# Kernel tuning notes

Measured on AMD Instinct MI355X. Metric: run time of the kernel, lower is better.

Reference implementation:

```python
import jax, jax.numpy as jnp
import numpy as np

B, N, D, H, TV, COND, BLK = 2, 1024, 1024, 16, 256, 1024, 16
HD = D // H  # 64
S = 2 * N    # total sequence [xt|x0]
EPS = 1e-5


def _ln(x, w):
    # bd3lm LayerNorm: no bias, weight multiply after normalization
    mu = jnp.mean(x, axis=-1, keepdims=True)
    var = jnp.mean(jnp.square(x - mu), axis=-1, keepdims=True)
    return (x - mu) * jax.lax.rsqrt(var + EPS) * w


def _rotate_half(u):
    u1, u2 = jnp.split(u, 2, axis=-1)
    return jnp.concatenate([-u2, u1], axis=-1)


def _apply_rotary(qkv, cos, sin):
    # qkv: (B, n, 3, H, HD); cos/sin: (1, n, 3, 1, HD) with identity on the v slot
    return qkv * cos + _rotate_half(qkv) * sin


def setup_inputs() -> dict:
    key = jax.random.key(0)
    ks = jax.random.split(key, 20)
    inp = {}
    inp['x'] = jax.random.normal(ks[0], (B, S, D), jnp.float32)
    inp['c'] = jax.random.normal(ks[1], (B, COND), jnp.float32)
    inp['encoder_out'] = jax.random.normal(ks[2], (B, TV, D), jnp.float32)
    # encoder padding mask: True = valid
    lengths = jax.random.randint(ks[3], (B,), TV // 2, TV + 1)
    inp['encoder_mask'] = jnp.arange(TV)[None, :] < lengths[:, None]
    # BD3LM block-causal mask over [xt|x0], shape (2N, 2N)
    bt = jnp.arange(N) // BLK
    M11 = bt[:, None] == bt[None, :]   # xt attends xt within same block
    M12 = bt[None, :] < bt[:, None]    # xt attends x0 of strictly earlier blocks
    M21 = jnp.zeros((N, N), bool)      # x0 does not attend xt
    M22 = bt[None, :] <= bt[:, None]   # x0 attends x0 block-causally
    inp['mask'] = jnp.concatenate([
        jnp.concatenate([M11, M12], axis=1),
        jnp.concatenate([M21, M22], axis=1)], axis=0)
    # rotary tables (SEDD-style), identity on v slot
    inv_freq = 1.0 / (10000.0 ** (jnp.arange(0, HD, 2, dtype=jnp.float32) / HD))
    freqs = jnp.outer(jnp.arange(N, dtype=jnp.float32), inv_freq)  # (N, HD/2)
    emb = jnp.concatenate([freqs, freqs], axis=-1)                 # (N, HD)
    cqk, sqk = jnp.cos(emb), jnp.sin(emb)
    inp['cos'] = jnp.stack([cqk, cqk, jnp.ones_like(cqk)], axis=1)[None, :, :, None, :]
    inp['sin'] = jnp.stack([sqk, sqk, jnp.zeros_like(sqk)], axis=1)[None, :, :, None, :]
    # parameters (torch Linear convention: W is (out, in), y = x @ W.T)
    sc = 0.02
    inp['ln1_w'] = jnp.ones((D,), jnp.float32)
    inp['W_qkv'] = jax.random.normal(ks[4], (3 * D, D), jnp.float32) * sc
    inp['W_attn_out'] = jax.random.normal(ks[5], (D, D), jnp.float32) * sc
    inp['ca_ln_w'] = jnp.ones((D,), jnp.float32)
    inp['ca_Wq'] = jax.random.normal(ks[6], (D, D), jnp.float32) * sc
    inp['ca_Wkv'] = jax.random.normal(ks[7], (2 * D, D), jnp.float32) * sc
    inp['ca_Wo'] = jax.random.normal(ks[8], (D, D), jnp.float32) * sc
    inp['ln2_w'] = jnp.ones((D,), jnp.float32)
    inp['W_mlp1'] = jax.random.normal(ks[9], (4 * D, D), jnp.float32) * sc
    inp['b_mlp1'] = jnp.zeros((4 * D,), jnp.float32)
    inp['W_mlp2'] = jax.random.normal(ks[10], (D, 4 * D), jnp.float32) * sc
    inp['b_mlp2'] = jnp.zeros((D,), jnp.float32)
    # adaLN (zero-init in the module; use small random weights for a non-trivial baseline)
    inp['W_ada'] = jax.random.normal(ks[11], (6 * D, COND), jnp.float32) * sc
    inp['b_ada'] = jax.random.normal(ks[12], (6 * D,), jnp.float32) * sc
    return inp


def _forward(x, c, encoder_out, encoder_mask, mask, cos, sin, ln1_w, W_qkv,
             W_attn_out, ca_ln_w, ca_Wq, ca_Wkv, ca_Wo, ln2_w, W_mlp1, b_mlp1,
             W_mlp2, b_mlp2, W_ada, b_ada):
    inv_sqrt_d = 1.0 / jnp.sqrt(jnp.float32(HD))
    ada = c @ W_ada.T + b_ada
    sh_msa, sc_msa, g_msa, sh_mlp, sc_mlp, g_mlp = [
        a[:, None, :] for a in jnp.split(ada, 6, axis=-1)]
    x_skip = x
    x_norm = _ln(x, ln1_w) * (1.0 + sc_msa) + sh_msa
    # qkv + rotary applied separately to xt and x0 halves (same positions 0..N-1)
    qkv = (x_norm @ W_qkv.T).reshape(B, S, 3, H, HD)
    qkv = jnp.concatenate([
        _apply_rotary(qkv[:, :N], cos, sin),
        _apply_rotary(qkv[:, N:], cos, sin)], axis=1)
    q, k, v = qkv[:, :, 0], qkv[:, :, 1], qkv[:, :, 2]  # (B, S, H, HD)
    # block-causal self-attention
    scores = jnp.einsum('bqhd,bkhd->bhqk', q, k) * inv_sqrt_d
    scores = jnp.where(mask[None, None, :, :], scores, jnp.finfo(scores.dtype).min)
    attn = jax.nn.softmax(scores, axis=-1)
    x_attn = jnp.einsum('bhqk,bkhd->bqhd', attn, v).reshape(B, S, D)
    # fused bias-dropout-add-scale (inference: scale * x + residual)
    x = g_msa * (x_attn @ W_attn_out.T) + x_skip
    # cross-attention to visual features
    res = x
    xn = _ln(x, ca_ln_w)
    qc = (xn @ ca_Wq.T).reshape(B, S, H, HD)
    kv = (encoder_out @ ca_Wkv.T).reshape(B, TV, 2, H, HD)
    kc, vc = kv[:, :, 0], kv[:, :, 1]
    cs = jnp.einsum('bqhd,bkhd->bhqk', qc, kc) * inv_sqrt_d
    cs = jnp.where(encoder_mask[:, None, None, :], cs, jnp.finfo(cs.dtype).min)
    ca = jax.nn.softmax(cs, axis=-1)
    co = jnp.einsum('bhqk,bkhd->bqhd', ca, vc).reshape(B, S, D)
    x = res + co @ ca_Wo.T
    # adaLN-modulated MLP (GELU tanh)
    h = _ln(x, ln2_w) * (1.0 + sc_mlp) + sh_mlp
    h = jax.nn.gelu(h @ W_mlp1.T + b_mlp1, approximate=True)
    return g_mlp * (h @ W_mlp2.T + b_mlp2) + x


def reference(x, c, encoder_out, encoder_mask, mask, cos, sin, ln1_w, W_qkv,
              W_attn_out, ca_ln_w, ca_Wq, ca_Wkv, ca_Wo, ln2_w, W_mlp1, b_mlp1,
              W_mlp2, b_mlp2, W_ada, b_ada):
    return _forward(x, c, encoder_out, encoder_mask, mask, cos, sin, ln1_w,
                    W_qkv, W_attn_out, ca_ln_w, ca_Wq, ca_Wkv, ca_Wo, ln2_w,
                    W_mlp1, b_mlp1, W_mlp2, b_mlp2, W_ada, b_ada)
```

## Files before the change

kernel.cpp:

```cpp
#include <hip/hip_runtime.h>
#include <hip/hip_bf16.h>

typedef __bf16 bf16x8 __attribute__((ext_vector_type(8)));
typedef __bf16 bf16x4 __attribute__((ext_vector_type(4)));
typedef float f32x4 __attribute__((ext_vector_type(4)));

typedef const __attribute__((address_space(1))) unsigned int* gas_t;
typedef __attribute__((address_space(3))) unsigned int* las_t;

__device__ __forceinline__ void gl_lds16(const void* g, void* l) {
    __builtin_amdgcn_global_load_lds((gas_t)g, (las_t)l, 16, 0, 0);
}

__device__ __forceinline__ float gelu_f(float u) {
    return u / (1.f + __expf(-1.5957691216057308f * (u + 0.044715f * u * u * u)));
}

struct CastArgs {
    const float4* src[8];
    __bf16* dst[8];
    int n4[8];
};
__global__ __launch_bounds__(256) void castmulti(CastArgs a) {
    int seg = blockIdx.y;
    const float4* src = a.src[seg];
    __bf16* dst = a.dst[seg];
    int n4 = a.n4[seg];
    for (int i = blockIdx.x * 256 + threadIdx.x; i < n4; i += 512 * 256) {
        float4 v = src[i];
        bf16x4 o;
        o[0] = (__bf16)v.x; o[1] = (__bf16)v.y; o[2] = (__bf16)v.z; o[3] = (__bf16)v.w;
        *(bf16x4*)(dst + (size_t)i * 4) = o;
    }
}

__global__ __launch_bounds__(256) void ada_kernel(const float* __restrict__ c, const float* __restrict__ W,
                                                  const float* __restrict__ bias, float* __restrict__ ada) {
    int o = blockIdx.x * 4 + (threadIdx.x >> 6);
    int lane = threadIdx.x & 63;
    int b = o / 6144, n = o % 6144;
    const float* cr = c + b * 1024;
    const float* wr = W + (size_t)n * 1024;
    float s = 0.f;
    #pragma unroll
    for (int i = 0; i < 16; ++i) s += cr[lane + i * 64] * wr[lane + i * 64];
    #pragma unroll
    for (int off = 1; off < 64; off <<= 1) s += __shfl_xor(s, off, 64);
    if (lane == 0) ada[o] = s + bias[n];
}

__global__ __launch_bounds__(256) void ln_kernel(const float* __restrict__ x, const float* __restrict__ w,
                                                 const float* __restrict__ ada, int sc_off, int sh_off,
                                                 int has_mod, __bf16* __restrict__ out) {
    int m = blockIdx.x;
    int b = m >> 11;
    int t = threadIdx.x;
    const float* xr = x + (size_t)m * 1024;
    float4 v = *(const float4*)(xr + t * 4);
    float s = v.x + v.y + v.z + v.w;
    float sq = v.x * v.x + v.y * v.y + v.z * v.z + v.w * v.w;
    #pragma unroll
    for (int off = 1; off < 64; off <<= 1) { s += __shfl_xor(s, off, 64); sq += __shfl_xor(sq, off, 64); }
    __shared__ float red[8];
    int wv = t >> 6, lane = t & 63;
    if (lane == 0) { red[wv] = s; red[4 + wv] = sq; }
    __syncthreads();
    s = red[0] + red[1] + red[2] + red[3];
    sq = red[4] + red[5] + red[6] + red[7];
    float mu = s * (1.f / 1024.f);
    float var = sq * (1.f / 1024.f) - mu * mu;
    float rs = rsqrtf(var + 1e-5f);
    const float* sc = ada + b * 6144 + sc_off;
    const float* sh = ada + b * 6144 + sh_off;
    float vv[4] = {v.x, v.y, v.z, v.w};
    #pragma unroll
    for (int i = 0; i < 4; ++i) {
        int d = t * 4 + i;
        float val = (vv[i] - mu) * rs * w[d];
        if (has_mod) val = val * (1.f + sc[d]) + sh[d];
        out[(size_t)m * 1024 + d] = (__bf16)val;
    }
}

__global__ __launch_bounds__(256) void rotary_kernel(const __bf16* __restrict__ qkv,
                                                     const float* __restrict__ cosp, const float* __restrict__ sinp,
                                                     __bf16* __restrict__ q, __bf16* __restrict__ k,
                                                     __bf16* __restrict__ v) {
    int m = blockIdx.y;
    int col = blockIdx.x * 256 + threadIdx.x;
    int tt = col >> 10;
    int hd = col & 1023;
    int h = hd >> 6, d = hd & 63;
    int b = m >> 11, s = m & 2047;
    int p = s & 1023;
    float u = (float)qkv[(size_t)m * 3072 + col];
    float res;
    if (tt < 2) {
        float cs = cosp[p * 192 + tt * 64 + d];
        float sn = sinp[p * 192 + tt * 64 + d];
        float prt = (float)qkv[(size_t)m * 3072 + (col ^ 32)];
        float rot = (d < 32) ? -prt : prt;
        res = u * cs + rot * sn;
        if (tt == 0) res *= 0.125f;
    } else {
        res = u;
    }
    size_t oi = ((size_t)(b * 16 + h) * 2048 + s) * 64 + d;
    __bf16* dst = (tt == 0) ? q : (tt == 1) ? k : v;
    dst[oi] = (__bf16)res;
}

__global__ __launch_bounds__(512) void gemm512(
    const __bf16* __restrict__ A, const __bf16* __restrict__ Bw,
    void* __restrict__ Cout, float* __restrict__ part,
    int M, int N, int K, int ksplit,
    const float* __restrict__ bias,
    const float* __restrict__ gate,
    const float* __restrict__ resid,
    int do_gelu, int out_bf16, float scale) {
    __shared__ __align__(16) __bf16 As[128 * 32];
    __shared__ __align__(16) __bf16 Bs[128 * 32];
    int t = threadIdx.x;
    int wv = t >> 6, lane = t & 63;
    int lrow = lane & 15, quad = lane >> 4;
    int m0 = blockIdx.y * 128, n0 = blockIdx.x * 128;
    int Ks = K / ksplit;
    int kbase = blockIdx.z * Ks;
    int wm = (wv >> 1) * 32, wn = (wv & 1) * 64;
    f32x4 acc[2][4] = {};
    const __bf16* Ag = A + (size_t)(m0 + wv * 16 + (lane >> 2)) * K + kbase + (lane & 3) * 8;
    const __bf16* Bg = Bw + (size_t)(n0 + wv * 16 + (lane >> 2)) * K + kbase + (lane & 3) * 8;
    __bf16* Asw = As + wv * 512;
    __bf16* Bsw = Bs + wv * 512;
    for (int k0 = 0; k0 < Ks; k0 += 32) {
        gl_lds16(Ag + k0, Asw);
        gl_lds16(Bg + k0, Bsw);
        __syncthreads();
        bf16x8 af[2], bfr[4];
        #pragma unroll
        for (int i = 0; i < 2; ++i) af[i] = *(const bf16x8*)(As + (wm + i * 16 + lrow) * 32 + quad * 8);
        #pragma unroll
        for (int j = 0; j < 4; ++j) bfr[j] = *(const bf16x8*)(Bs + (wn + j * 16 + lrow) * 32 + quad * 8);
        #pragma unroll
        for (int i = 0; i < 2; ++i)
            #pragma unroll
            for (int j = 0; j < 4; ++j)
                acc[i][j] = __builtin_amdgcn_mfma_f32_16x16x32_bf16(af[i], bfr[j], acc[i][j], 0, 0, 0);
        __syncthreads();
    }
    if (ksplit > 1) {
        float* pp = part + (size_t)blockIdx.z * M * N;
        #pragma unroll
        for (int i = 0; i < 2; ++i)
            #pragma unroll
            for (int j = 0; j < 4; ++j)
                #pragma unroll
                for (int r = 0; r < 4; ++r) {
                    int gm = m0 + wm + i * 16 + quad * 4 + r;
                    int gn = n0 + wn + j * 16 + lrow;
                    pp[(size_t)gm * N + gn] = acc[i][j][r] * scale;
                }
        return;
    }
    #pragma unroll
    for (int i = 0; i < 2; ++i) {
        #pragma unroll
        for (int j = 0; j < 4; ++j) {
            #pragma unroll
            for (int r = 0; r < 4; ++r) {
                int gm = m0 + wm + i * 16 + quad * 4 + r;
                int gn = n0 + wn + j * 16 + lrow;
                float val = acc[i][j][r] * scale;
                if (bias) val += bias[gn];
                if (do_gelu) val = gelu_f(val);
                if (gate) val *= gate[(gm >> 11) * 6144 + gn];
                if (resid) val += resid[(size_t)gm * N + gn];
                if (out_bf16) ((__bf16*)Cout)[(size_t)gm * N + gn] = (__bf16)val;
                else ((float*)Cout)[(size_t)gm * N + gn] = val;
            }
        }
    }
}

__global__ __launch_bounds__(256) void reduce2(
    const float4* __restrict__ p0, const float4* __restrict__ p1,
    const float* __restrict__ bias, const float* __restrict__ gate,
    const float* __restrict__ resid, float* __restrict__ out, int n4tot) {
    int i = blockIdx.x * 256 + threadIdx.x;
    if (i >= n4tot) return;
    float4 a = p0[i], b = p1[i];
    int idx = i * 4;
    int n = idx & 1023;
    int bb = idx >> 21;
    float4 bs = *(const float4*)(bias + n);
    float4 g = *(const float4*)(gate + bb * 6144 + n);
    float4 rr = ((const float4*)resid)[i];
    float4 o;
    o.x = g.x * (a.x + b.x + bs.x) + rr.x;
    o.y = g.y * (a.y + b.y + bs.y) + rr.y;
    o.z = g.z * (a.z + b.z + bs.z) + rr.z;
    o.w = g.w * (a.w + b.w + bs.w) + rr.w;
    ((float4*)out)[i] = o;
}

__global__ __launch_bounds__(256) void attn_kernel(
    const __bf16* __restrict__ qp, const __bf16* __restrict__ kp, const __bf16* __restrict__ vp,
    __bf16* __restrict__ op, const void* __restrict__ emask,
    int Sk, int mode,
    long qB, long qH, int qR,
    long kB, long kH, int kR,
    long vB, long vH, int vR,
    long oB, long oH, int oR) {
    __shared__ __bf16 Qs[64][72];
    __shared__ __bf16 Ks[64][72];
    __shared__ __bf16 Vt[64][72];
    __shared__ __bf16 Ps[4][16][72];
    int bh = blockIdx.y;
    int b = bh >> 4, h = bh & 15;
    int s0 = blockIdx.x * 64;
    int t = threadIdx.x;
    int wv = t >> 6, lane = t & 63;
    int lrow = lane & 15, quad = lane >> 4;
    const __bf16* qbase = qp + (size_t)b * qB + (size_t)h * qH;
    const __bf16* kbase = kp + (size_t)b * kB + (size_t)h * kH;
    const __bf16* vbase = vp + (size_t)b * vB + (size_t)h * vH;

    #pragma unroll
    for (int rep = 0; rep < 2; ++rep) {
        int g = t + rep * 256;
        int row = g >> 3, sg = g & 7;
        *(uint4*)(&Qs[row][sg * 8]) = *(const uint4*)(qbase + (size_t)(s0 + row) * qR + sg * 8);
    }
    bool m_is_i32 = false;
    if (mode == 1) m_is_i32 = (((const unsigned char*)emask)[1] == 0);

    float mrun[4], lrun[4];
    #pragma unroll
    for (int r = 0; r < 4; ++r) { mrun[r] = -1e30f; lrun[r] = 0.f; }
    f32x4 oacc[4] = {};

    int nt;
    if (mode == 1) nt = Sk >> 6;
    else nt = (s0 < 1024) ? (s0 / 64 + 2) : ((s0 - 1024) / 64 + 1);

    for (int ti = 0; ti < nt; ++ti) {
        int kb;
        if (mode == 1) kb = ti * 64;
        else if (s0 < 1024) kb = (ti == 0) ? s0 : 1024 + (ti - 1) * 64;
        else kb = 1024 + ti * 64;
        __syncthreads();
        #pragma unroll
        for (int rep = 0; rep < 2; ++rep) {
            int g = t + rep * 256;
            int row = g >> 3, sg = g & 7;
            *(uint4*)(&Ks[row][sg * 8]) = *(const uint4*)(kbase + (size_t)(kb + row) * kR + sg * 8);
        }
        {
            int j2 = (t & 31) * 2, dc = t >> 5;
            bf16x8 va = *(const bf16x8*)(vbase + (size_t)(kb + j2) * vR + dc * 8);
            bf16x8 vb2 = *(const bf16x8*)(vbase + (size_t)(kb + j2 + 1) * vR + dc * 8);
            #pragma unroll
            for (int i = 0; i < 8; ++i) {
                Vt[dc * 8 + i][j2] = va[i];
                Vt[dc * 8 + i][j2 + 1] = vb2[i];
            }
        }
        __syncthreads();
        f32x4 sacc[4] = {};
        #pragma unroll
        for (int ks = 0; ks < 64; ks += 32) {
            bf16x8 aq = *(const bf16x8*)(&Qs[wv * 16 + lrow][ks + quad * 8]);
            #pragma unroll
            for (int cc = 0; cc < 4; ++cc) {
                bf16x8 bk = *(const bf16x8*)(&Ks[cc * 16 + lrow][ks + quad * 8]);
                sacc[cc] = __builtin_amdgcn_mfma_f32_16x16x32_bf16(aq, bk, sacc[cc], 0, 0, 0);
            }
        }
        #pragma unroll
        for (int cc = 0; cc < 4; ++cc) {
            int kg = kb + cc * 16 + lrow;
            if (mode == 1) {
                bool visc = m_is_i32 ? (((const int*)emask)[b * Sk + kg] != 0)
                                     : (((const unsigned char*)emask)[b * Sk + kg] != 0);
                if (!visc) {
                    #pragma unroll
                    for (int r = 0; r < 4; ++r) sacc[cc][r] = -1e30f;
                }
            } else {
                #pragma unroll
                for (int r = 0; r < 4; ++r) {
                    int qg = s0 + wv * 16 + quad * 4 + r;
                    bool qh = qg < 1024, kh = kg < 1024;
                    bool vis;
                    if (qh && kh) vis = (qg >> 4) == (kg >> 4);
                    else if (qh) vis = ((kg - 1024) >> 4) < (qg >> 4);
                    else if (kh) vis = false;
                    else vis = ((kg - 1024) >> 4) <= ((qg - 1024) >> 4);
                    if (!vis) sacc[cc][r] = -1e30f;
                }
            }
        }
        #pragma unroll
        for (int r = 0; r < 4; ++r) {
            float mt = fmaxf(fmaxf(sacc[0][r], sacc[1][r]), fmaxf(sacc[2][r], sacc[3][r]));
            #pragma unroll
            for (int off = 1; off < 16; off <<= 1) mt = fmaxf(mt, __shfl_xor(mt, off, 64));
            float mnew = fmaxf(mrun[r], mt);
            float alpha = __expf(mrun[r] - mnew);
            float psum = 0.f;
            #pragma unroll
            for (int cc = 0; cc < 4; ++cc) {
                float pv = __expf(sacc[cc][r] - mnew);
                sacc[cc][r] = pv;
                psum += pv;
            }
            #pragma unroll
            for (int off = 1; off < 16; off <<= 1) psum += __shfl_xor(psum, off, 64);
            lrun[r] = lrun[r] * alpha + psum;
            mrun[r] = mnew;
            #pragma unroll
            for (int cc = 0; cc < 4; ++cc) oacc[cc][r] *= alpha;
            #pragma unroll
            for (int cc = 0; cc < 4; ++cc)
                Ps[wv][quad * 4 + r][cc * 16 + lrow] = (__bf16)sacc[cc][r];
        }
        __syncthreads();
        #pragma unroll
        for (int ks = 0; ks < 64; ks += 32) {
            bf16x8 ap = *(const bf16x8*)(&Ps[wv][lrow][ks + quad * 8]);
            #pragma unroll
            for (int cc = 0; cc < 4; ++cc) {
                bf16x8 bv = *(const bf16x8*)(&Vt[cc * 16 + lrow][ks + quad * 8]);
                oacc[cc] = __builtin_amdgcn_mfma_f32_16x16x32_bf16(ap, bv, oacc[cc], 0, 0, 0);
            }
        }
    }
    __bf16* obase = op + (size_t)b * oB + (size_t)h * oH;
    #pragma unroll
    for (int cc = 0; cc < 4; ++cc) {
        #pragma unroll
        for (int r = 0; r < 4; ++r) {
            int qg = s0 + wv * 16 + quad * 4 + r;
            obase[(size_t)qg * oR + cc * 16 + lrow] = (__bf16)(oacc[cc][r] / lrun[r]);
        }
    }
}


extern "C" void kernel_launch(void* const* d_in, const int* in_sizes, int n_in,
                              void* d_out, int out_size, void* d_ws, size_t ws_size,
                              hipStream_t stream) {
    const float* x      = (const float*)d_in[0];
    const float* c      = (const float*)d_in[1];
    const float* enc    = (const float*)d_in[2];
    const void*  emask  = d_in[3];
    const float* cosp   = (const float*)d_in[5];
    const float* sinp   = (const float*)d_in[6];
    const float* ln1_w  = (const float*)d_in[7];
    const float* W_qkv  = (const float*)d_in[8];
    const float* W_ao   = (const float*)d_in[9];
    const float* ca_ln_w= (const float*)d_in[10];
    const float* ca_Wq  = (const float*)d_in[11];
    const float* ca_Wkv = (const float*)d_in[12];
    const float* ca_Wo  = (const float*)d_in[13];
    const float* ln2_w  = (const float*)d_in[14];
    const float* W_m1   = (const float*)d_in[15];
    const float* b_m1   = (const float*)d_in[16];
    const float* W_m2   = (const float*)d_in[17];
    const float* b_m2   = (const float*)d_in[18];
    const float* W_ada  = (const float*)d_in[19];
    const float* b_ada  = (const float*)d_in[20];
    float* out = (float*)d_out;

    char* ws = (char*)d_ws;
    const size_t MB = 1ull << 20;
    float*  ada   = (float*)(ws + 0);
    __bf16* encb  = (__bf16*)(ws + 1 * MB);
    __bf16* xn    = (__bf16*)(ws + 2 * MB);
    float*  xA    = (float*)(ws + 10 * MB);
    float*  xB    = (float*)(ws + 26 * MB);
    float*  part  = (float*)(ws + 42 * MB);
    __bf16* qkvb  = (__bf16*)(ws + 42 * MB);
    __bf16* qb    = (__bf16*)(ws + 74 * MB);
    __bf16* kbuf  = (__bf16*)(ws + 82 * MB);
    __bf16* vbuf  = (__bf16*)(ws + 90 * MB);
    __bf16* xat   = (__bf16*)(ws + 98 * MB);
    __bf16* hbuf  = (__bf16*)(ws + 98 * MB);
    __bf16* wqkv  = (__bf16*)(ws + 130 * MB);
    __bf16* wao   = (__bf16*)(ws + 136 * MB);
    __bf16* wcaq  = (__bf16*)(ws + 138 * MB);
    __bf16* wcakv = (__bf16*)(ws + 140 * MB);
    __bf16* wcao  = (__bf16*)(ws + 144 * MB);
    __bf16* wm1   = (__bf16*)(ws + 146 * MB);
    __bf16* wm2   = (__bf16*)(ws + 154 * MB);

    CastArgs ca;
    ca.src[0] = (const float4*)enc;    ca.dst[0] = encb;  ca.n4[0] = 131072;
    ca.src[1] = (const float4*)W_qkv;  ca.dst[1] = wqkv;  ca.n4[1] = 786432;
    ca.src[2] = (const float4*)W_ao;   ca.dst[2] = wao;   ca.n4[2] = 262144;
    ca.src[3] = (const float4*)ca_Wq;  ca.dst[3] = wcaq;  ca.n4[3] = 262144;
    ca.src[4] = (const float4*)ca_Wkv; ca.dst[4] = wcakv; ca.n4[4] = 524288;
    ca.src[5] = (const float4*)ca_Wo;  ca.dst[5] = wcao;  ca.n4[5] = 262144;
    ca.src[6] = (const float4*)W_m1;   ca.dst[6] = wm1;   ca.n4[6] = 1048576;
    ca.src[7] = (const float4*)W_m2;   ca.dst[7] = wm2;   ca.n4[7] = 1048576;
    castmulti<<<dim3(512, 8), 256, 0, stream>>>(ca);
    ada_kernel<<<3072, 256, 0, stream>>>(c, W_ada, b_ada, ada);
    ln_kernel<<<4096, 256, 0, stream>>>(x, ln1_w, ada, 1024, 0, 1, xn);
    gemm512<<<dim3(24, 32, 1), 512, 0, stream>>>(xn, wqkv, qkvb, nullptr, 4096, 3072, 1024, 1,
        nullptr, nullptr, nullptr, 0, 1, 1.f);
    rotary_kernel<<<dim3(12, 4096), 256, 0, stream>>>(qkvb, cosp, sinp, qb, kbuf, vbuf);
    attn_kernel<<<dim3(32, 32), 256, 0, stream>>>(qb, kbuf, vbuf, xat, nullptr, 2048, 0,
        2097152L, 131072L, 64, 2097152L, 131072L, 64, 2097152L, 131072L, 64,
        2097152L, 64L, 1024);
    gemm512<<<dim3(8, 32, 1), 512, 0, stream>>>(xat, wao, xA, nullptr, 4096, 1024, 1024, 1,
        nullptr, ada + 2048, x, 0, 0, 1.f);
    ln_kernel<<<4096, 256, 0, stream>>>(xA, ca_ln_w, ada, 0, 0, 0, xn);
    gemm512<<<dim3(8, 32, 1), 512, 0, stream>>>(xn, wcaq, qb, nullptr, 4096, 1024, 1024, 1,
        nullptr, nullptr, nullptr, 0, 1, 0.125f);
    gemm512<<<dim3(16, 4, 1), 512, 0, stream>>>(encb, wcakv, kbuf, nullptr, 512, 2048, 1024, 1,
        nullptr, nullptr, nullptr, 0, 1, 1.f);
    attn_kernel<<<dim3(32, 32), 256, 0, stream>>>(qb, kbuf, kbuf + 1024, vbuf, emask, 256, 1,
        2097152L, 64L, 1024, 524288L, 64L, 2048, 524288L, 64L, 2048,
        2097152L, 64L, 1024);
    gemm512<<<dim3(8, 32, 1), 512, 0, stream>>>(vbuf, wcao, xB, nullptr, 4096, 1024, 1024, 1,
        nullptr, nullptr, xA, 0, 0, 1.f);
    ln_kernel<<<4096, 256, 0, stream>>>(xB, ln2_w, ada, 4096, 3072, 1, xn);
    gemm512<<<dim3(32, 32, 1), 512, 0, stream>>>(xn, wm1, hbuf, nullptr, 4096, 4096, 1024, 1,
        b_m1, nullptr, nullptr, 1, 1, 1.f);
    gemm512<<<dim3(8, 32, 2), 512, 0, stream>>>(hbuf, wm2, nullptr, part, 4096, 1024, 4096, 2,
        nullptr, nullptr, nullptr, 0, 0, 1.f);
    reduce2<<<4096, 256, 0, stream>>>((const float4*)part, (const float4*)(part + (size_t)4096 * 1024),
        b_m2, ada + 5120, xB, out, 1048576);
}
```

Measured before the change: 615.9 us.

## Fuse rotary into QKV GEMM epilogue and transpose attention MFMA layout

```diff
diff --git a/kernel.cpp b/kernel.cpp
--- a/kernel.cpp
+++ b/kernel.cpp
@@ -3,6 +3,7 @@
 
 typedef __bf16 bf16x8 __attribute__((ext_vector_type(8)));
 typedef __bf16 bf16x4 __attribute__((ext_vector_type(4)));
+typedef __bf16 bf16x2 __attribute__((ext_vector_type(2)));
 typedef float f32x4 __attribute__((ext_vector_type(4)));
 
 typedef const __attribute__((address_space(1))) unsigned int* gas_t;
@@ -82,34 +83,6 @@
     }
 }
 
-__global__ __launch_bounds__(256) void rotary_kernel(const __bf16* __restrict__ qkv,
-                                                     const float* __restrict__ cosp, const float* __restrict__ sinp,
-                                                     __bf16* __restrict__ q, __bf16* __restrict__ k,
-                                                     __bf16* __restrict__ v) {
-    int m = blockIdx.y;
-    int col = blockIdx.x * 256 + threadIdx.x;
-    int tt = col >> 10;
-    int hd = col & 1023;
-    int h = hd >> 6, d = hd & 63;
-    int b = m >> 11, s = m & 2047;
-    int p = s & 1023;
-    float u = (float)qkv[(size_t)m * 3072 + col];
-    float res;
-    if (tt < 2) {
-        float cs = cosp[p * 192 + tt * 64 + d];
-        float sn = sinp[p * 192 + tt * 64 + d];
-        float prt = (float)qkv[(size_t)m * 3072 + (col ^ 32)];
-        float rot = (d < 32) ? -prt : prt;
-        res = u * cs + rot * sn;
-        if (tt == 0) res *= 0.125f;
-    } else {
-        res = u;
-    }
-    size_t oi = ((size_t)(b * 16 + h) * 2048 + s) * 64 + d;
-    __bf16* dst = (tt == 0) ? q : (tt == 1) ? k : v;
-    dst[oi] = (__bf16)res;
-}
-
 __global__ __launch_bounds__(512) void gemm512(
     const __bf16* __restrict__ A, const __bf16* __restrict__ Bw,
     void* __restrict__ Cout, float* __restrict__ part,
@@ -117,7 +90,10 @@
     const float* __restrict__ bias,
     const float* __restrict__ gate,
     const float* __restrict__ resid,
-    int do_gelu, int out_bf16, float scale) {
+    int do_gelu, int out_bf16, float scale,
+    const float* __restrict__ cosp, const float* __restrict__ sinp,
+    __bf16* __restrict__ rq, __bf16* __restrict__ rk, __bf16* __restrict__ rv_,
+    int rot) {
     __shared__ __align__(16) __bf16 As[128 * 32];
     __shared__ __align__(16) __bf16 Bs[128 * 32];
     int t = threadIdx.x;
@@ -148,6 +124,32 @@
                 acc[i][j] = __builtin_amdgcn_mfma_f32_16x16x32_bf16(af[i], bfr[j], acc[i][j], 0, 0, 0);
         __syncthreads();
     }
+    if (rot) {
+        #pragma unroll
+        for (int i = 0; i < 2; ++i)
+            #pragma unroll
+            for (int j = 0; j < 4; ++j)
+                #pragma unroll
+                for (int r = 0; r < 4; ++r) {
+                    int gm = m0 + wm + i * 16 + quad * 4 + r;
+                    int gn = n0 + wn + j * 16 + lrow;
+                    int tt = gn >> 10, hd = gn & 1023;
+                    int hh = hd >> 6, d = hd & 63;
+                    int bb = gm >> 11, s = gm & 2047, p = s & 1023;
+                    float val = acc[i][j][r];
+                    if (tt < 2) {
+                        float cs = cosp[p * 192 + tt * 64 + d];
+                        float sn = sinp[p * 192 + tt * 64 + d];
+                        float prt = acc[i][j ^ 2][r];
+                        float rvv = (d < 32) ? -prt : prt;
+                        val = val * cs + rvv * sn;
+                        if (tt == 0) val *= 0.125f;
+                    }
+                    __bf16* dst = (tt == 0) ? rq : (tt == 1) ? rk : rv_;
+                    dst[((size_t)(bb * 16 + hh) * 2048 + s) * 64 + d] = (__bf16)val;
+                }
+        return;
+    }
     if (ksplit > 1) {
         float* pp = part + (size_t)blockIdx.z * M * N;
         #pragma unroll
@@ -215,6 +217,7 @@
     __shared__ __bf16 Ks[64][72];
     __shared__ __bf16 Vt[64][72];
     __shared__ __bf16 Ps[4][16][72];
+    __shared__ float Msk[64];
     int bh = blockIdx.y;
     int b = bh >> 4, h = bh & 15;
     int s0 = blockIdx.x * 64;
@@ -234,9 +237,12 @@
     bool m_is_i32 = false;
     if (mode == 1) m_is_i32 = (((const unsigned char*)emask)[1] == 0);
 
-    float mrun[4], lrun[4];
-    #pragma unroll
-    for (int r = 0; r < 4; ++r) { mrun[r] = -1e30f; lrun[r] = 0.f; }
+    int qg = s0 + wv * 16 + lrow;
+    bool qh = qg < 1024;
+    int qb1 = qg >> 4;
+    int qb2 = (qg - 1024) >> 4;
+
+    float mrun = -1e30f, lrun = 0.f;
     f32x4 oacc[4] = {};
 
     int nt;
@@ -261,88 +267,96 @@
             bf16x8 vb2 = *(const bf16x8*)(vbase + (size_t)(kb + j2 + 1) * vR + dc * 8);
             #pragma unroll
             for (int i = 0; i < 8; ++i) {
-                Vt[dc * 8 + i][j2] = va[i];
-                Vt[dc * 8 + i][j2 + 1] = vb2[i];
+                bf16x2 pr; pr[0] = va[i]; pr[1] = vb2[i];
+                *(bf16x2*)(&Vt[dc * 8 + i][j2]) = pr;
             }
+        }
+        if (mode == 1 && t < 64) {
+            int kg = kb + t;
+            bool vis = m_is_i32 ? (((const int*)emask)[b * Sk + kg] != 0)
+                                : (((const unsigned char*)emask)[b * Sk + kg] != 0);
+            Msk[t] = vis ? 0.f : -1e30f;
         }
         __syncthreads();
         f32x4 sacc[4] = {};
         #pragma unroll
         for (int ks = 0; ks < 64; ks += 32) {
-            bf16x8 aq = *(const bf16x8*)(&Qs[wv * 16 + lrow][ks + quad * 8]);
+            bf16x8 bq = *(const bf16x8*)(&Qs[wv * 16 + lrow][ks + quad * 8]);
             #pragma unroll
             for (int cc = 0; cc < 4; ++cc) {
-                bf16x8 bk = *(const bf16x8*)(&Ks[cc * 16 + lrow][ks + quad * 8]);
-                sacc[cc] = __builtin_amdgcn_mfma_f32_16x16x32_bf16(aq, bk, sacc[cc], 0, 0, 0);
+                bf16x8 ak = *(const bf16x8*)(&Ks[cc * 16 + lrow][ks + quad * 8]);
+                sacc[cc] = __builtin_amdgcn_mfma_f32_16x16x32_bf16(ak, bq, sacc[cc], 0, 0, 0);
             }
         }
-        #pragma unroll
-        for (int cc = 0; cc < 4; ++cc) {
-            int kg = kb + cc * 16 + lrow;
-            if (mode == 1) {
-                bool visc = m_is_i32 ? (((const int*)emask)[b * Sk + kg] != 0)
-                                     : (((const unsigned char*)emask)[b * Sk + kg] != 0);
-                if (!visc) {
-                    #pragma unroll
-                    for (int r = 0; r < 4; ++r) sacc[cc][r] = -1e30f;
-                }
-            } else {
+        float mloc = -1e30f;
+        if (mode == 1) {
+            #pragma unroll
+            for (int cc = 0; cc < 4; ++cc)
                 #pragma unroll
                 for (int r = 0; r < 4; ++r) {
-                    int qg = s0 + wv * 16 + quad * 4 + r;
-                    bool qh = qg < 1024, kh = kg < 1024;
+                    sacc[cc][r] += Msk[cc * 16 + quad * 4 + r];
+                    mloc = fmaxf(mloc, sacc[cc][r]);
+                }
+        } else {
+            #pragma unroll
+            for (int cc = 0; cc < 4; ++cc)
+                #pragma unroll
+                for (int r = 0; r < 4; ++r) {
+                    int kg = kb + cc * 16 + quad * 4 + r;
+                    bool kh = kg < 1024;
                     bool vis;
-                    if (qh && kh) vis = (qg >> 4) == (kg >> 4);
-                    else if (qh) vis = ((kg - 1024) >> 4) < (qg >> 4);
-                    else if (kh) vis = false;
-                    else vis = ((kg - 1024) >> 4) <= ((qg - 1024) >> 4);
+                    if (qh) vis = kh ? ((kg >> 4) == qb1) : (((kg - 1024) >> 4) < qb1);
+                    else    vis = kh ? false : (((kg - 1024) >> 4) <= qb2);
                     if (!vis) sacc[cc][r] = -1e30f;
+                    mloc = fmaxf(mloc, sacc[cc][r]);
                 }
-            }
-        }
-        #pragma unroll
-        for (int r = 0; r < 4; ++r) {
-            float mt = fmaxf(fmaxf(sacc[0][r], sacc[1][r]), fmaxf(sacc[2][r], sacc[3][r]));
-            #pragma unroll
-            for (int off = 1; off < 16; off <<= 1) mt = fmaxf(mt, __shfl_xor(mt, off, 64));
-            float mnew = fmaxf(mrun[r], mt);
-            float alpha = __expf(mrun[r] - mnew);
-            float psum = 0.f;
-            #pragma unroll
-            for (int cc = 0; cc < 4; ++cc) {
+        }
+        mloc = fmaxf(mloc, __shfl_xor(mloc, 16, 64));
+        mloc = fmaxf(mloc, __shfl_xor(mloc, 32, 64));
+        float mnew = fmaxf(mrun, mloc);
+        float alpha = __expf(mrun - mnew);
+        float ps = 0.f;
+        #pragma unroll
+        for (int cc = 0; cc < 4; ++cc)
+            #pragma unroll
+            for (int r = 0; r < 4; ++r) {
                 float pv = __expf(sacc[cc][r] - mnew);
                 sacc[cc][r] = pv;
-                psum += pv;
+                ps += pv;
             }
-            #pragma unroll
-            for (int off = 1; off < 16; off <<= 1) psum += __shfl_xor(psum, off, 64);
-            lrun[r] = lrun[r] * alpha + psum;
-            mrun[r] = mnew;
-            #pragma unroll
-            for (int cc = 0; cc < 4; ++cc) oacc[cc][r] *= alpha;
-            #pragma unroll
-            for (int cc = 0; cc < 4; ++cc)
-                Ps[wv][quad * 4 + r][cc * 16 + lrow] = (__bf16)sacc[cc][r];
-        }
-        __syncthreads();
+        ps += __shfl_xor(ps, 16, 64);
+        ps += __shfl_xor(ps, 32, 64);
+        lrun = lrun * alpha + ps;
+        mrun = mnew;
+        #pragma unroll
+        for (int i = 0; i < 4; ++i)
+            #pragma unroll
+            for (int r = 0; r < 4; ++r) oacc[i][r] *= alpha;
+        #pragma unroll
+        for (int cc = 0; cc < 4; ++cc) {
+            bf16x4 pk;
+            #pragma unroll
+            for (int r = 0; r < 4; ++r) pk[r] = (__bf16)sacc[cc][r];
+            *(bf16x4*)(&Ps[wv][lrow][cc * 16 + quad * 4]) = pk;
+        }
         #pragma unroll
         for (int ks = 0; ks < 64; ks += 32) {
-            bf16x8 ap = *(const bf16x8*)(&Ps[wv][lrow][ks + quad * 8]);
-            #pragma unroll
-            for (int cc = 0; cc < 4; ++cc) {
-                bf16x8 bv = *(const bf16x8*)(&Vt[cc * 16 + lrow][ks + quad * 8]);
-                oacc[cc] = __builtin_amdgcn_mfma_f32_16x16x32_bf16(ap, bv, oacc[cc], 0, 0, 0);
+            bf16x8 bp = *(const bf16x8*)(&Ps[wv][lrow][ks + quad * 8]);
+            #pragma unroll
+            for (int i = 0; i < 4; ++i) {
+                bf16x8 av = *(const bf16x8*)(&Vt[i * 16 + lrow][ks + quad * 8]);
+                oacc[i] = __builtin_amdgcn_mfma_f32_16x16x32_bf16(av, bp, oacc[i], 0, 0, 0);
             }
         }
     }
     __bf16* obase = op + (size_t)b * oB + (size_t)h * oH;
-    #pragma unroll
-    for (int cc = 0; cc < 4; ++cc) {
-        #pragma unroll
-        for (int r = 0; r < 4; ++r) {
-            int qg = s0 + wv * 16 + quad * 4 + r;
-            obase[(size_t)qg * oR + cc * 16 + lrow] = (__bf16)(oacc[cc][r] / lrun[r]);
-        }
+    float rl = 1.f / lrun;
+    #pragma unroll
+    for (int i = 0; i < 4; ++i) {
+        bf16x4 ov;
+        #pragma unroll
+        for (int r = 0; r < 4; ++r) ov[r] = (__bf16)(oacc[i][r] * rl);
+        *(bf16x4*)(obase + (size_t)qg * oR + i * 16 + quad * 4) = ov;
     }
 }
 
@@ -380,7 +394,6 @@
     float*  xA    = (float*)(ws + 10 * MB);
     float*  xB    = (float*)(ws + 26 * MB);
     float*  part  = (float*)(ws + 42 * MB);
-    __bf16* qkvb  = (__bf16*)(ws + 42 * MB);
     __bf16* qb    = (__bf16*)(ws + 74 * MB);
     __bf16* kbuf  = (__bf16*)(ws + 82 * MB);
     __bf16* vbuf  = (__bf16*)(ws + 90 * MB);
@@ -406,29 +419,28 @@
     castmulti<<<dim3(512, 8), 256, 0, stream>>>(ca);
     ada_kernel<<<3072, 256, 0, stream>>>(c, W_ada, b_ada, ada);
     ln_kernel<<<4096, 256, 0, stream>>>(x, ln1_w, ada, 1024, 0, 1, xn);
-    gemm512<<<dim3(24, 32, 1), 512, 0, stream>>>(xn, wqkv, qkvb, nullptr, 4096, 3072, 1024, 1,
-        nullptr, nullptr, nullptr, 0, 1, 1.f);
-    rotary_kernel<<<dim3(12, 4096), 256, 0, stream>>>(qkvb, cosp, sinp, qb, kbuf, vbuf);
+    gemm512<<<dim3(24, 32, 1), 512, 0, stream>>>(xn, wqkv, nullptr, nullptr, 4096, 3072, 1024, 1,
+        nullptr, nullptr, nullptr, 0, 1, 1.f, cosp, sinp, qb, kbuf, vbuf, 1);
     attn_kernel<<<dim3(32, 32), 256, 0, stream>>>(qb, kbuf, vbuf, xat, nullptr, 2048, 0,
         2097152L, 131072L, 64, 2097152L, 131072L, 64, 2097152L, 131072L, 64,
         2097152L, 64L, 1024);
     gemm512<<<dim3(8, 32, 1), 512, 0, stream>>>(xat, wao, xA, nullptr, 4096, 1024, 1024, 1,
-        nullptr, ada + 2048, x, 0, 0, 1.f);
+        nullptr, ada + 2048, x, 0, 0, 1.f, nullptr, nullptr, nullptr, nullptr, nullptr, 0);
     ln_kernel<<<4096, 256, 0, stream>>>(xA, ca_ln_w, ada, 0, 0, 0, xn);
     gemm512<<<dim3(8, 32, 1), 512, 0, stream>>>(xn, wcaq, qb, nullptr, 4096, 1024, 1024, 1,
-        nullptr, nullptr, nullptr, 0, 1, 0.125f);
+        nullptr, nullptr, nullptr, 0, 1, 0.125f, nullptr, nullptr, nullptr, nullptr, nullptr, 0);
     gemm512<<<dim3(16, 4, 1), 512, 0, stream>>>(encb, wcakv, kbuf, nullptr, 512, 2048, 1024, 1,
-        nullptr, nullptr, nullptr, 0, 1, 1.f);
+        nullptr, nullptr, nullptr, 0, 1, 1.f, nullptr, nullptr, nullptr, nullptr, nullptr, 0);
     attn_kernel<<<dim3(32, 32), 256, 0, stream>>>(qb, kbuf, kbuf + 1024, vbuf, emask, 256, 1,
         2097152L, 64L, 1024, 524288L, 64L, 2048, 524288L, 64L, 2048,
         2097152L, 64L, 1024);
     gemm512<<<dim3(8, 32, 1), 512, 0, stream>>>(vbuf, wcao, xB, nullptr, 4096, 1024, 1024, 1,
-        nullptr, nullptr, xA, 0, 0, 1.f);
+        nullptr, nullptr, xA, 0, 0, 1.f, nullptr, nullptr, nullptr, nullptr, nullptr, 0);
     ln_kernel<<<4096, 256, 0, stream>>>(xB, ln2_w, ada, 4096, 3072, 1, xn);
     gemm512<<<dim3(32, 32, 1), 512, 0, stream>>>(xn, wm1, hbuf, nullptr, 4096, 4096, 1024, 1,
-        b_m1, nullptr, nullptr, 1, 1, 1.f);
+        b_m1, nullptr, nullptr, 1, 1, 1.f, nullptr, nullptr, nullptr, nullptr, nullptr, 0);
     gemm512<<<dim3(8, 32, 2), 512, 0, stream>>>(hbuf, wm2, nullptr, part, 4096, 1024, 4096, 2,
-        nullptr, nullptr, nullptr, 0, 0, 1.f);
+        nullptr, nullptr, nullptr, 0, 0, 1.f, nullptr, nullptr, nullptr, nullptr, nullptr, 0);
     reduce2<<<4096, 256, 0, stream>>>((const float4*)part, (const float4*)(part + (size_t)4096 * 1024),
         b_m2, ada + 5120, xB, out, 1048576);
 }
```

Result: faster. 590.4 us (-4.1%).
